# Performance work log

Hardware: AMD Instinct MI355X
Metric: run time of the kernel (lower is better)

## Reference

```python
import jax, jax.numpy as jnp
import numpy as np
from jax import lax

STRIDE = 4

def grid_sample_nearest(feat, grid):
    # feat: (B, C, H, W); grid: (B, Ho, Wo, 2) normalized to [-1, 1], align_corners=True,
    # mode='nearest', padding_mode='zeros' (matches torch.nn.functional.grid_sample).
    B, C, H, W = feat.shape
    gx = (grid[..., 0] + 1.0) * 0.5 * (W - 1)
    gy = (grid[..., 1] + 1.0) * 0.5 * (H - 1)
    ix = jnp.round(gx).astype(jnp.int32)  # round-half-to-even == std::nearbyint
    iy = jnp.round(gy).astype(jnp.int32)
    valid = (ix >= 0) & (ix < W) & (iy >= 0) & (iy < H)
    ixc = jnp.clip(ix, 0, W - 1)
    iyc = jnp.clip(iy, 0, H - 1)
    out = jax.vmap(lambda f, y, x: f[:, y, x])(feat, iyc, ixc)  # (B, C, Ho, Wo)
    return out * valid[:, None, :, :].astype(feat.dtype)

def unfold_s(x, s):
    # F.unfold(x, kernel=(s,s), stride=s): (n,c,h,w) -> (n, c*s*s, h//s * w//s)
    n, c, h, w = x.shape
    h4, w4 = h // s, w // s
    x = x.reshape(n, c, h4, s, w4, s).transpose(0, 1, 3, 5, 2, 4)  # (n,c,kh,kw,h4,w4)
    return x.reshape(n, c * s * s, h4 * w4)

def fold_s(x, s, c, h, w):
    # F.fold, kernel=(s,s), stride=s (non-overlapping): (n, c*s*s, h4*w4) -> (n,c,h,w)
    n = x.shape[0]
    h4, w4 = h // s, w // s
    x = x.reshape(n, c, s, s, h4, w4).transpose(0, 1, 4, 2, 5, 3)  # (n,c,h4,kh,w4,kw)
    return x.reshape(n, c, h, w)

def _normalize(x, axis):
    return x / jnp.maximum(jnp.linalg.norm(x, axis=axis, keepdims=True), 1e-12)

def ltam_forward(curr_feat, index_feat_set_s1, anchor_feat, sparse_feat_set_s1,
                 sparse_feat_set_s2, sparse_feat_set_s3, location_feat,
                 fusion_w, fusion_b):
    s = STRIDE
    n, c, h, w = anchor_feat.shape
    t = sparse_feat_set_s1.shape[1]
    h4, w4 = h // s, w // s
    feat_len = c * s * s
    feat_num = h4 * w4

    # build normalized nearest-sampling grid from location map
    gf = location_feat.reshape(n, t, 2, h4, w4).transpose(0, 1, 3, 4, 2)  # (n,t,h4,w4,2)
    gx = 2.0 * gf[..., 0] / max(w4 - 1, 1) - 1.0
    gy = 2.0 * gf[..., 1] / max(h4 - 1, 1) - 1.0
    grid = jnp.stack([gx, gy], axis=-1).reshape(n * t, h4, w4, 2)

    def warp(fs):
        return grid_sample_nearest(fs.reshape(n * t, feat_len, h4, w4), grid)

    out_s1 = warp(sparse_feat_set_s1)   # (n*t, feat_len, h4, w4)
    out_s2 = warp(sparse_feat_set_s2)
    out_s3 = warp(sparse_feat_set_s3)
    idx_s1 = warp(index_feat_set_s1)

    # current-frame patch tokens, L2-normalized
    cf = unfold_s(curr_feat, s).transpose(0, 2, 1)          # (n, feat_num, feat_len)
    cf = _normalize(cf, axis=2)

    # index tokens per frame, L2-normalized, correlate with current tokens
    idx_tok = idx_s1.reshape(n, t, feat_len, feat_num).transpose(0, 3, 1, 2)  # (n,feat_num,t,feat_len)
    idx_tok = _normalize(idx_tok, axis=3)
    matrix_index = jnp.einsum('nptf,npf->npt', idx_tok, cf)  # (n, feat_num, t)

    corr_soft = jnp.max(matrix_index, axis=2)                # (n, feat_num)
    corr_index = jnp.argmax(matrix_index, axis=2)            # (n, feat_num)

    corr_soft_map = fold_s(jnp.broadcast_to(corr_soft[:, None, :], (n, feat_len, feat_num)),
                           s, c, h, w)                       # (n, c, h, w)

    def gather_fold(o):
        o = o.reshape(n, t, feat_len, feat_num)
        idx = jnp.broadcast_to(corr_index[:, None, None, :], (n, 1, feat_len, feat_num))
        g = jnp.take_along_axis(o, idx, axis=1)[:, 0]        # (n, feat_len, feat_num)
        return fold_s(g, s, c, h, w)

    f1 = gather_fold(out_s1)
    f2 = gather_fold(out_s2)
    f3 = gather_fold(out_s3)

    out = jnp.concatenate([f1, f2, f3], axis=1)              # (n, 3c, h, w)
    out = lax.conv_general_dilated(out, fusion_w, (1, 1), ((1, 1), (1, 1)),
                                   dimension_numbers=('NCHW', 'OIHW', 'NCHW'))
    out = out + fusion_b[None, :, None, None]
    out = out * corr_soft_map + anchor_feat
    return out

def setup_inputs() -> dict:
    key = jax.random.key(0)
    ks = jax.random.split(key, 10)
    n, t, c, h, w, s = 1, 4, 128, 192, 192, STRIDE
    h4, w4 = h // s, w // s
    feat_len = c * s * s
    inp = {
        'curr_feat': jax.random.normal(ks[0], (n, c, h, w), jnp.float32),
        'index_feat_set_s1': jax.random.normal(ks[1], (n, t, feat_len, h4, w4), jnp.float32),
        'anchor_feat': jax.random.normal(ks[2], (n, c, h, w), jnp.float32),
        'sparse_feat_set_s1': jax.random.normal(ks[3], (n, t, feat_len, h4, w4), jnp.float32),
        'sparse_feat_set_s2': jax.random.normal(ks[4], (n, t, feat_len, h4, w4), jnp.float32),
        'sparse_feat_set_s3': jax.random.normal(ks[5], (n, t, feat_len, h4, w4), jnp.float32),
        # unnormalized pixel coordinates in [0, dim-1] (h4 == w4 here)
        'location_feat': jax.random.uniform(ks[6], (n, 2 * t, h4, w4), jnp.float32) * (w4 - 1),
        'fusion_w': jax.random.normal(ks[7], (c, 3 * c, 3, 3), jnp.float32) * 0.02,
        'fusion_b': jax.random.normal(ks[8], (c,), jnp.float32) * 0.02,
    }
    return inp

def reference(curr_feat, index_feat_set_s1, anchor_feat, sparse_feat_set_s1,
              sparse_feat_set_s2, sparse_feat_set_s3, location_feat,
              fusion_w, fusion_b):
    return ltam_forward(curr_feat, index_feat_set_s1, anchor_feat, sparse_feat_set_s1,
                        sparse_feat_set_s2, sparse_feat_set_s3, location_feat,
                        fusion_w, fusion_b)
```

## Files before the change

kernel.cpp:

```cpp
#include <hip/hip_runtime.h>
#include <hip/hip_bf16.h>
#include <math.h>

#define T_FRAMES 4
#define C 128
#define H 192
#define W 192
#define H4 48
#define W4 48
#define FEAT_LEN 2048
#define FEAT_NUM 2304
#define HW (H*W)
#define NCH 384
#define KTOT 3456
#define NSTEP 54
#define PPX 194

typedef __bf16 bf16x8 __attribute__((ext_vector_type(8)));
typedef float f32x4 __attribute__((ext_vector_type(4)));

__device__ __forceinline__ void gl16(const void* gp, void* ldsbase) {
    __builtin_amdgcn_global_load_lds(
        (const __attribute__((address_space(1))) void*)gp,
        (__attribute__((address_space(3))) void*)ldsbase, 16, 0, 0);
}

__device__ __forceinline__ void sample_loc(const float* __restrict__ loc, int k, int p,
                                           int& iy, int& ix, int& valid) {
    float gfx = loc[(2*k+0)*FEAT_NUM + p];
    float gfy = loc[(2*k+1)*FEAT_NUM + p];
    float gx = 2.0f*gfx/47.0f - 1.0f;
    float gy = 2.0f*gfy/47.0f - 1.0f;
    float fx = (gx + 1.0f)*0.5f*47.0f;
    float fy = (gy + 1.0f)*0.5f*47.0f;
    int jx = (int)rintf(fx);
    int jy = (int)rintf(fy);
    valid = (jx >= 0 && jx < W4 && jy >= 0 && jy < H4) ? 1 : 0;
    ix = min(max(jx, 0), W4-1);
    iy = min(max(jy, 0), H4-1);
}

__global__ __launch_bounds__(256) void k_tr(const float* __restrict__ src,
                                            float* __restrict__ dst) {
    __shared__ float lds[64*65];
    int p0 = blockIdx.x*64, f0 = blockIdx.y*64, k = blockIdx.z;
    const float* s = src + (size_t)k*FEAT_LEN*FEAT_NUM;
    float* d = dst + (size_t)k*FEAT_NUM*FEAT_LEN;
    int tid = threadIdx.x;
    int pq = (tid & 15)*4, fr = tid >> 4;
#pragma unroll
    for (int i = 0; i < 4; ++i) {
        int fl = fr + i*16;
        float4 v = *(const float4*)&s[(size_t)(f0+fl)*FEAT_NUM + p0 + pq];
        lds[fl*65 + pq + 0] = v.x;
        lds[fl*65 + pq + 1] = v.y;
        lds[fl*65 + pq + 2] = v.z;
        lds[fl*65 + pq + 3] = v.w;
    }
    __syncthreads();
    int f4 = (tid & 15)*4, pb = tid >> 4;
#pragma unroll
    for (int i = 0; i < 4; ++i) {
        int pl2 = pb + i*16;
        float4 v = { lds[(f4+0)*65 + pl2], lds[(f4+1)*65 + pl2],
                     lds[(f4+2)*65 + pl2], lds[(f4+3)*65 + pl2] };
        *(float4*)&d[(size_t)(p0+pl2)*FEAT_LEN + f0 + f4] = v;
    }
}

__global__ __launch_bounds__(256) void k_trs(const float* __restrict__ s1,
                                             const float* __restrict__ s2,
                                             const float* __restrict__ s3,
                                             ushort* __restrict__ spT) {
    __shared__ float lds[64*65];
    int p0 = blockIdx.x*64, f0 = blockIdx.y*64;
    int z = blockIdx.z;
    int set = z >> 2, k = z & 3;
    const float* src = (set == 0) ? s1 : ((set == 1) ? s2 : s3);
    const float* s = src + (size_t)k*FEAT_LEN*FEAT_NUM;
    int tid = threadIdx.x;
    int pq = (tid & 15)*4, fr = tid >> 4;
#pragma unroll
    for (int i = 0; i < 4; ++i) {
        int fl = fr + i*16;
        float4 v = *(const float4*)&s[(size_t)(f0+fl)*FEAT_NUM + p0 + pq];
        lds[fl*65 + pq + 0] = v.x;
        lds[fl*65 + pq + 1] = v.y;
        lds[fl*65 + pq + 2] = v.z;
        lds[fl*65 + pq + 3] = v.w;
    }
    __syncthreads();
    int fo = (tid & 7)*8, pr = tid >> 3;
#pragma unroll
    for (int i = 0; i < 2; ++i) {
        int row = pr + i*32;
        ushort vv[8];
#pragma unroll
        for (int j = 0; j < 8; ++j) {
            __hip_bfloat16 b = __float2bfloat16(lds[(fo+j)*65 + row]);
            vv[j] = *(ushort*)&b;
        }
        uint4 pk;
        pk.x = (uint)vv[0] | ((uint)vv[1] << 16);
        pk.y = (uint)vv[2] | ((uint)vv[3] << 16);
        pk.z = (uint)vv[4] | ((uint)vv[5] << 16);
        pk.w = (uint)vv[6] | ((uint)vv[7] << 16);
        *(uint4*)(spT + ((size_t)z*FEAT_NUM + p0 + row)*FEAT_LEN + f0 + fo) = pk;
    }
}

__global__ __launch_bounds__(256) void k_gather2(const ushort* __restrict__ spT,
                                                 const float* __restrict__ loc,
                                                 const int* __restrict__ corr_index,
                                                 ushort* __restrict__ cat) {
    __shared__ ushort tok[3*FEAT_LEN];
    int p = blockIdx.x;
    int y4 = p / W4, x4 = p - y4*W4;
    int tid = threadIdx.x;
    int k = corr_index[p];
    int iy, ix, valid;
    sample_loc(loc, k, p, iy, ix, valid);
    int sp = iy*W4 + ix;

#pragma unroll
    for (int j = 0; j < 3; ++j) {
        int idx = j*256 + tid;
        int set = idx >> 8, off = (idx & 255)*8;
        uint4 v = {0u,0u,0u,0u};
        if (valid)
            v = *(const uint4*)(spT + ((size_t)(set*4 + k)*FEAT_NUM + sp)*FEAT_LEN + off);
        *(uint4*)(tok + set*FEAT_LEN + off) = v;
    }
    __syncthreads();

#pragma unroll
    for (int j = 0; j < 3; ++j) {
        int idx = j*256 + tid;
        int px16 = idx / 48, oct = idx - px16*48;
        int ky = px16 >> 2, kx = px16 & 3;
        int y = y4*4 + ky, x = x4*4 + kx;
        int set = oct >> 4, c0 = (oct & 15)*8;
        int sub = (ky << 2) + kx;
        ushort vv[8];
#pragma unroll
        for (int e = 0; e < 8; ++e) vv[e] = tok[set*FEAT_LEN + ((c0 + e) << 4) + sub];
        uint4 pk;
        pk.x = (uint)vv[0] | ((uint)vv[1] << 16);
        pk.y = (uint)vv[2] | ((uint)vv[3] << 16);
        pk.z = (uint)vv[4] | ((uint)vv[5] << 16);
        pk.w = (uint)vv[6] | ((uint)vv[7] << 16);
        *(uint4*)(cat + ((size_t)(y+1)*PPX + (x+1))*NCH + set*128 + c0) = pk;
    }
}

__global__ __launch_bounds__(256) void k_corr2(const float* __restrict__ curr,
                                               const float* __restrict__ idxT,
                                               const float* __restrict__ loc,
                                               int* __restrict__ corr_index,
                                               float* __restrict__ corr_soft) {
    int p = blockIdx.x;
    int y4 = p / W4, x4 = p - y4*W4;
    int tid = threadIdx.x;

    int iy[T_FRAMES], ix[T_FRAMES], valid[T_FRAMES];
    const float* tok[T_FRAMES];
#pragma unroll
    for (int k = 0; k < T_FRAMES; ++k) {
        sample_loc(loc, k, p, iy[k], ix[k], valid[k]);
        tok[k] = idxT + ((size_t)k*FEAT_NUM + iy[k]*W4 + ix[k])*FEAT_LEN;
    }

    float ss_cf = 0.f;
    float dotk[T_FRAMES] = {0.f,0.f,0.f,0.f};
    float ssk[T_FRAMES]  = {0.f,0.f,0.f,0.f};
    int ybase = y4*4, xbase = x4*4;

#pragma unroll
    for (int it = 0; it < 2; ++it) {
        int f4 = (tid + it*256)*4;
        int cc = f4 >> 4, kh = (f4 >> 2) & 3;
        float4 cf = *(const float4*)&curr[cc*HW + (ybase+kh)*W + xbase];
        ss_cf += cf.x*cf.x + cf.y*cf.y + cf.z*cf.z + cf.w*cf.w;
#pragma unroll
        for (int k = 0; k < T_FRAMES; ++k) {
            if (valid[k]) {
                float4 v = *(const float4*)&tok[k][f4];
                dotk[k] += cf.x*v.x + cf.y*v.y + cf.z*v.z + cf.w*v.w;
                ssk[k]  += v.x*v.x + v.y*v.y + v.z*v.z + v.w*v.w;
            }
        }
    }

    float vals[9] = {ss_cf, dotk[0],dotk[1],dotk[2],dotk[3], ssk[0],ssk[1],ssk[2],ssk[3]};
#pragma unroll
    for (int j = 0; j < 9; ++j) {
        float v = vals[j];
#pragma unroll
        for (int off = 32; off > 0; off >>= 1) v += __shfl_xor(v, off, 64);
        vals[j] = v;
    }
    __shared__ float red[4][9];
    int wave = tid >> 6, lane = tid & 63;
    if (lane == 0) {
#pragma unroll
        for (int j = 0; j < 9; ++j) red[wave][j] = vals[j];
    }
    __syncthreads();
    if (tid == 0) {
        float tot[9];
#pragma unroll
        for (int j = 0; j < 9; ++j) tot[j] = red[0][j]+red[1][j]+red[2][j]+red[3][j];
        float ncf = fmaxf(sqrtf(tot[0]), 1e-12f);
        float best = -1e30f; int bestk = 0;
#pragma unroll
        for (int k = 0; k < T_FRAMES; ++k) {
            float nk = fmaxf(sqrtf(tot[5+k]), 1e-12f);
            float m = tot[1+k] / (nk * ncf);
            if (m > best) { best = m; bestk = k; }
        }
        corr_index[p] = bestk;
        corr_soft[p]  = best;
    }
}

__global__ __launch_bounds__(256) void k_corr(const float* __restrict__ curr,
                                              const float* __restrict__ idxf,
                                              const float* __restrict__ loc,
                                              int* __restrict__ corr_index,
                                              float* __restrict__ corr_soft) {
    int p = blockIdx.x;
    int y4 = p / W4, x4 = p - y4*W4;
    int tid = threadIdx.x;

    int iy[T_FRAMES], ix[T_FRAMES], valid[T_FRAMES];
#pragma unroll
    for (int k = 0; k < T_FRAMES; ++k) sample_loc(loc, k, p, iy[k], ix[k], valid[k]);

    float ss_cf = 0.f;
    float dotk[T_FRAMES] = {0.f,0.f,0.f,0.f};
    float ssk[T_FRAMES]  = {0.f,0.f,0.f,0.f};

    int ybase = y4*4, xbase = x4*4;
    for (int f = tid; f < FEAT_LEN; f += 256) {
        int cc = f >> 4;
        int kh = (f >> 2) & 3;
        int kw = f & 3;
        float cf = curr[cc*HW + (ybase+kh)*W + (xbase+kw)];
        ss_cf += cf*cf;
#pragma unroll
        for (int k = 0; k < T_FRAMES; ++k) {
            float v = 0.f;
            if (valid[k]) v = idxf[(k*FEAT_LEN + f)*FEAT_NUM + iy[k]*W4 + ix[k]];
            dotk[k] += cf*v;
            ssk[k]  += v*v;
        }
    }

    float vals[9] = {ss_cf, dotk[0],dotk[1],dotk[2],dotk[3], ssk[0],ssk[1],ssk[2],ssk[3]};
#pragma unroll
    for (int j = 0; j < 9; ++j) {
        float v = vals[j];
#pragma unroll
        for (int off = 32; off > 0; off >>= 1) v += __shfl_xor(v, off, 64);
        vals[j] = v;
    }
    __shared__ float red[4][9];
    int wave = tid >> 6, lane = tid & 63;
    if (lane == 0) {
#pragma unroll
        for (int j = 0; j < 9; ++j) red[wave][j] = vals[j];
    }
    __syncthreads();
    if (tid == 0) {
        float tot[9];
#pragma unroll
        for (int j = 0; j < 9; ++j) tot[j] = red[0][j]+red[1][j]+red[2][j]+red[3][j];
        float ncf = fmaxf(sqrtf(tot[0]), 1e-12f);
        float best = -1e30f; int bestk = 0;
#pragma unroll
        for (int k = 0; k < T_FRAMES; ++k) {
            float nk = fmaxf(sqrtf(tot[5+k]), 1e-12f);
            float m = tot[1+k] / (nk * ncf);
            if (m > best) { best = m; bestk = k; }
        }
        corr_index[p] = bestk;
        corr_soft[p]  = best;
    }
}

__global__ __launch_bounds__(256) void k_wconv(const float* __restrict__ w,
                                               ushort* __restrict__ wt2) {
    int gid = blockIdx.x*256 + threadIdx.x;
    if (gid >= 128*KTOT) return;
    int e  = gid & 7;
    int l  = (gid >> 3) & 63;
    int g  = (gid >> 9) & 7;
    int kkstep = gid >> 12;
    int kk = kkstep & 1, step = kkstep >> 1;
    int lx = l & 15, lg = l >> 4;
    int col = g*16 + lx;
    int chunk = step / 9, tap = step - chunk*9;
    int ci = chunk*64 + kk*32 + lg*8 + e;
    __hip_bfloat16 b = __float2bfloat16(w[(col*NCH + ci)*9 + tap]);
    wt2[gid] = *(ushort*)&b;
}

__global__ __launch_bounds__(256) void k_border(ushort* __restrict__ cat) {
    int gid = blockIdx.x*256 + threadIdx.x;
    if (gid >= 772*48) return;
    int oct = gid % 48, bp = gid / 48;
    int ypad, xpad;
    if (bp < 194)      { ypad = 0;        xpad = bp; }
    else if (bp < 388) { ypad = 193;      xpad = bp - 194; }
    else if (bp < 580) { ypad = bp - 387; xpad = 0; }
    else               { ypad = bp - 579; xpad = 193; }
    uint4 z = {0u,0u,0u,0u};
    *(uint4*)(cat + (ypad*PPX + xpad)*NCH + oct*8) = z;
}

__global__ __launch_bounds__(256) void k_gather(const float* __restrict__ s1,
                                                const float* __restrict__ s2,
                                                const float* __restrict__ s3,
                                                const float* __restrict__ loc,
                                                const int* __restrict__ corr_index,
                                                ushort* __restrict__ cat) {
    int gid = blockIdx.x*256 + threadIdx.x;
    if (gid >= HW*48) return;
    int oct = gid % 48, px = gid / 48;
    int x = px % W, y = px / W;
    int p = (y >> 2)*W4 + (x >> 2);
    int k = corr_index[p];
    int iy, ix, valid;
    sample_loc(loc, k, p, iy, ix, valid);
    int set = oct >> 4;
    int c0  = (oct & 15) * 8;
    int sub = ((y & 3) << 2) + (x & 3);
    ushort v[8];
#pragma unroll
    for (int e = 0; e < 8; ++e) v[e] = 0;
    if (valid) {
        const float* src = (set == 0) ? s1 : ((set == 1) ? s2 : s3);
        const float* sp = src + (size_t)k*FEAT_LEN*FEAT_NUM + iy*W4 + ix;
#pragma unroll
        for (int e = 0; e < 8; ++e) {
            int f = ((c0 + e) << 4) + sub;
            __hip_bfloat16 b = __float2bfloat16(sp[(size_t)f*FEAT_NUM]);
            v[e] = *(ushort*)&b;
        }
    }
    uint4 pk;
    pk.x = (uint)v[0] | ((uint)v[1] << 16);
    pk.y = (uint)v[2] | ((uint)v[3] << 16);
    pk.z = (uint)v[4] | ((uint)v[5] << 16);
    pk.w = (uint)v[6] | ((uint)v[7] << 16);
    *(uint4*)(cat + ((y+1)*PPX + (x+1))*NCH + oct*8) = pk;
}

__global__ __launch_bounds__(256, 2) void k_conv2(const ushort* __restrict__ cat,
                                                  const ushort* __restrict__ wt2,
                                                  const float* __restrict__ bias,
                                                  const float* __restrict__ corr_soft,
                                                  const float* __restrict__ anchor,
                                                  float* __restrict__ out) {
    __shared__ char smX[2][136*128];

    int tx = blockIdx.x, ty = blockIdx.y;
    int tid = threadIdx.x;
    int wave = tid >> 6, l = tid & 63;
    int lx = l & 15, lg = l >> 4;
    int co0w = wave * 32;
    int wbofs = (wave*64)*16;

    auto stageX = [&](int chunk, int b) {
        char* xb = (char*)smX[b];
#pragma unroll
        for (int q = 0; q < 4; ++q) {
            int idx = tid + q*256;
            int rc = idx >> 3, oct = idx & 7;
            int r = rc / 34, xp = rc - r*34;
            int octp = oct ^ (xp & 7);
            const ushort* gp = cat + ((size_t)(ty*2 + r)*PPX + (tx*32 + xp))*NCH
                               + chunk*64 + octp*8;
            gl16(gp, xb + q*256*16 + wbofs);
        }
        if (wave == 0) {
            int idx = 1024 + l;
            int rc = idx >> 3, oct = idx & 7;
            int xp = rc - 102;
            int octp = oct ^ (xp & 7);
            const ushort* gp = cat + ((size_t)(ty*2 + 3)*PPX + (tx*32 + xp))*NCH
                               + chunk*64 + octp*8;
            gl16(gp, xb + 1024*16);
        }
    };

    f32x4 acc[2][4];
#pragma unroll
    for (int mf = 0; mf < 2; ++mf)
#pragma unroll
        for (int nf = 0; nf < 4; ++nf) acc[mf][nf] = (f32x4){0.f,0.f,0.f,0.f};

    int pyv[4], pxxv[4];
#pragma unroll
    for (int nf = 0; nf < 4; ++nf) { int pxl = nf*16 + lx; pyv[nf] = pxl >> 5; pxxv[nf] = pxl & 31; }
    const ushort* wfb[2];
#pragma unroll
    for (int mf = 0; mf < 2; ++mf)
        wfb[mf] = wt2 + ((wave*2 + mf)*64 + l)*8;

    stageX(0, 0);
    __syncthreads();

    for (int chunk = 0; chunk < 6; ++chunk) {
        if (chunk < 5) stageX(chunk+1, (chunk+1) & 1);
        const char* Xb = smX[chunk & 1];
#pragma unroll
        for (int tap = 0; tap < 9; ++tap) {
            const int step = chunk*9 + tap;
            const int dy = tap/3 - 1, dx = tap%3 - 1;
            bf16x8 wf[2][2];
#pragma unroll
            for (int mf = 0; mf < 2; ++mf)
#pragma unroll
                for (int kk = 0; kk < 2; ++kk)
                    wf[mf][kk] = *(const bf16x8*)(wfb[mf] + (size_t)(step*2 + kk)*4096);
            int xrc[4], xsw[4];
#pragma unroll
            for (int nf = 0; nf < 4; ++nf) {
                int xp2 = pxxv[nf] + dx + 1;
                xrc[nf] = (pyv[nf] + dy + 1)*34 + xp2;
                xsw[nf] = (xp2 & 7) << 4;
            }
#pragma unroll
            for (int kk = 0; kk < 2; ++kk) {
                int kb = kk*64 + lg*16;
                bf16x8 xf[4];
#pragma unroll
                for (int nf = 0; nf < 4; ++nf)
                    xf[nf] = *(const bf16x8*)(Xb + xrc[nf]*128 + (kb ^ xsw[nf]));
#pragma unroll
                for (int mf = 0; mf < 2; ++mf)
#pragma unroll
                    for (int nf = 0; nf < 4; ++nf)
                        acc[mf][nf] = __builtin_amdgcn_mfma_f32_16x16x32_bf16(
                            wf[mf][kk], xf[nf], acc[mf][nf], 0, 0, 0);
            }
        }
        __syncthreads();
    }

    float cs[4]; int pixo[4];
#pragma unroll
    for (int nf = 0; nf < 4; ++nf) {
        int y = ty*2 + pyv[nf];
        int x = tx*32 + pxxv[nf];
        cs[nf] = corr_soft[(ty >> 1)*W4 + (x >> 2)];
        pixo[nf] = y*W + x;
    }
#pragma unroll
    for (int mf = 0; mf < 2; ++mf) {
#pragma unroll
        for (int j = 0; j < 4; ++j) {
            int co = co0w + mf*16 + lg*4 + j;
            float b = bias[co];
#pragma unroll
            for (int nf = 0; nf < 4; ++nf) {
                int o = co*HW + pixo[nf];
                out[o] = (acc[mf][nf][j] + b)*cs[nf] + anchor[o];
            }
        }
    }
}

extern "C" void kernel_launch(void* const* d_in, const int* in_sizes, int n_in,
                              void* d_out, int out_size, void* d_ws, size_t ws_size,
                              hipStream_t stream) {
    const float* curr   = (const float*)d_in[0];
    const float* idxf   = (const float*)d_in[1];
    const float* anchor = (const float*)d_in[2];
    const float* s1     = (const float*)d_in[3];
    const float* s2     = (const float*)d_in[4];
    const float* s3     = (const float*)d_in[5];
    const float* loc    = (const float*)d_in[6];
    const float* wgt    = (const float*)d_in[7];
    const float* bias   = (const float*)d_in[8];
    float* out = (float*)d_out;

    char* ws = (char*)d_ws;
    int*    corr_index = (int*)ws;
    float*  corr_soft  = (float*)(ws + 16384);
    ushort* wt2        = (ushort*)(ws + 32768);
    ushort* cat        = (ushort*)(ws + 917504);
    char*   big        = ws + 917504 + 28912128;
    float*  idxT       = (float*)big;
    ushort* spT        = (ushort*)big;
    const size_t SPT_BYTES  = (size_t)3*T_FRAMES*FEAT_NUM*FEAT_LEN*2;
    const size_t IDXT_BYTES = (size_t)T_FRAMES*FEAT_NUM*FEAT_LEN*4;
    const size_t NEED_A = 29829632 + (SPT_BYTES > IDXT_BYTES ? SPT_BYTES : IDXT_BYTES);
    const size_t NEED_B = 917504 + IDXT_BYTES;

    if (ws_size >= NEED_A) {
        hipLaunchKernelGGL(k_tr, dim3(36, 32, 4), dim3(256), 0, stream, idxf, idxT);
        hipLaunchKernelGGL(k_corr2, dim3(FEAT_NUM), dim3(256), 0, stream,
                           curr, idxT, loc, corr_index, corr_soft);
        hipLaunchKernelGGL(k_wconv, dim3((128*KTOT + 255)/256), dim3(256), 0, stream, wgt, wt2);
        hipLaunchKernelGGL(k_border, dim3((772*48 + 255)/256), dim3(256), 0, stream, cat);
        hipLaunchKernelGGL(k_trs, dim3(36, 32, 12), dim3(256), 0, stream, s1, s2, s3, spT);
        hipLaunchKernelGGL(k_gather2, dim3(FEAT_NUM), dim3(256), 0, stream,
                           spT, loc, corr_index, cat);
    } else {
        float*  idxT_b = (float*)(ws + 917504);
        ushort* cat_b  = (ushort*)(ws + 917504);
        if (ws_size >= NEED_B) {
            hipLaunchKernelGGL(k_tr, dim3(36, 32, 4), dim3(256), 0, stream, idxf, idxT_b);
            hipLaunchKernelGGL(k_corr2, dim3(FEAT_NUM), dim3(256), 0, stream,
                               curr, idxT_b, loc, corr_index, corr_soft);
        } else {
            hipLaunchKernelGGL(k_corr, dim3(FEAT_NUM), dim3(256), 0, stream,
                               curr, idxf, loc, corr_index, corr_soft);
        }
        hipLaunchKernelGGL(k_wconv, dim3((128*KTOT + 255)/256), dim3(256), 0, stream, wgt, wt2);
        hipLaunchKernelGGL(k_border, dim3((772*48 + 255)/256), dim3(256), 0, stream, cat_b);
        hipLaunchKernelGGL(k_gather, dim3((HW*48 + 255)/256), dim3(256), 0, stream,
                           s1, s2, s3, loc, corr_index, cat_b);
        hipLaunchKernelGGL(k_conv2, dim3(6, 96), dim3(256), 0, stream,
                           cat_b, wt2, bias, corr_soft, anchor, out);
        return;
    }
    hipLaunchKernelGGL(k_conv2, dim3(6, 96), dim3(256), 0, stream,
                       cat, wt2, bias, corr_soft, anchor, out);
}
```

Before: 202.6 us.

## Skip transposing feature rows that no sampling location references

A small kernel builds a per-frame bitmask of which source positions the nearest-sample grid actually hits. The correlation kernel records a second bitmask for the winning frame's positions. Both transpose kernels then skip writing rows whose position is not marked, which cuts global write traffic for the transposed index and sparse-feature buffers. This costs a memset, an extra tiny launch and atomics, and source reads still happen in full.

```diff
diff --git a/kernel.cpp b/kernel.cpp
--- a/kernel.cpp
+++ b/kernel.cpp
@@ -15,6 +15,7 @@
 #define KTOT 3456
 #define NSTEP 54
 #define PPX 194
+#define NBW 72
 
 typedef __bf16 bf16x8 __attribute__((ext_vector_type(8)));
 typedef float f32x4 __attribute__((ext_vector_type(4)));
@@ -40,8 +41,22 @@
     iy = min(max(jy, 0), H4-1);
 }
 
+__global__ __launch_bounds__(256) void k_needA(const float* __restrict__ loc,
+                                               uint* __restrict__ needA) {
+    int p = blockIdx.x*256 + threadIdx.x;
+    if (p >= FEAT_NUM) return;
+#pragma unroll
+    for (int k = 0; k < T_FRAMES; ++k) {
+        int iy, ix, valid;
+        sample_loc(loc, k, p, iy, ix, valid);
+        int sp = iy*W4 + ix;
+        atomicOr(&needA[k*NBW + (sp >> 5)], 1u << (sp & 31));
+    }
+}
+
 __global__ __launch_bounds__(256) void k_tr(const float* __restrict__ src,
-                                            float* __restrict__ dst) {
+                                            float* __restrict__ dst,
+                                            const uint* __restrict__ needA) {
     __shared__ float lds[64*65];
     int p0 = blockIdx.x*64, f0 = blockIdx.y*64, k = blockIdx.z;
     const float* s = src + (size_t)k*FEAT_LEN*FEAT_NUM;
@@ -62,16 +77,19 @@
 #pragma unroll
     for (int i = 0; i < 4; ++i) {
         int pl2 = pb + i*16;
+        int sp = p0 + pl2;
+        if (!(needA[k*NBW + (sp >> 5)] & (1u << (sp & 31)))) continue;
         float4 v = { lds[(f4+0)*65 + pl2], lds[(f4+1)*65 + pl2],
                      lds[(f4+2)*65 + pl2], lds[(f4+3)*65 + pl2] };
-        *(float4*)&d[(size_t)(p0+pl2)*FEAT_LEN + f0 + f4] = v;
+        *(float4*)&d[(size_t)sp*FEAT_LEN + f0 + f4] = v;
     }
 }
 
 __global__ __launch_bounds__(256) void k_trs(const float* __restrict__ s1,
                                              const float* __restrict__ s2,
                                              const float* __restrict__ s3,
-                                             ushort* __restrict__ spT) {
+                                             ushort* __restrict__ spT,
+                                             const uint* __restrict__ needB) {
     __shared__ float lds[64*65];
     int p0 = blockIdx.x*64, f0 = blockIdx.y*64;
     int z = blockIdx.z;
@@ -94,6 +112,8 @@
 #pragma unroll
     for (int i = 0; i < 2; ++i) {
         int row = pr + i*32;
+        int sp = p0 + row;
+        if (!(needB[k*NBW + (sp >> 5)] & (1u << (sp & 31)))) continue;
         ushort vv[8];
 #pragma unroll
         for (int j = 0; j < 8; ++j) {
@@ -105,7 +125,7 @@
         pk.y = (uint)vv[2] | ((uint)vv[3] << 16);
         pk.z = (uint)vv[4] | ((uint)vv[5] << 16);
         pk.w = (uint)vv[6] | ((uint)vv[7] << 16);
-        *(uint4*)(spT + ((size_t)z*FEAT_NUM + p0 + row)*FEAT_LEN + f0 + fo) = pk;
+        *(uint4*)(spT + ((size_t)z*FEAT_NUM + sp)*FEAT_LEN + f0 + fo) = pk;
     }
 }
 
@@ -157,7 +177,8 @@
                                                const float* __restrict__ idxT,
                                                const float* __restrict__ loc,
                                                int* __restrict__ corr_index,
-                                               float* __restrict__ corr_soft) {
+                                               float* __restrict__ corr_soft,
+                                               uint* __restrict__ needB) {
     int p = blockIdx.x;
     int y4 = p / W4, x4 = p - y4*W4;
     int tid = threadIdx.x;
@@ -220,6 +241,8 @@
         }
         corr_index[p] = bestk;
         corr_soft[p]  = best;
+        int spb = iy[bestk]*W4 + ix[bestk];
+        atomicOr(&needB[bestk*NBW + (spb >> 5)], 1u << (spb & 31));
     }
 }
 
@@ -488,6 +511,8 @@
 
     char* ws = (char*)d_ws;
     int*    corr_index = (int*)ws;
+    uint*   needA      = (uint*)(ws + 12288);
+    uint*   needB      = (uint*)(ws + 13696);
     float*  corr_soft  = (float*)(ws + 16384);
     ushort* wt2        = (ushort*)(ws + 32768);
     ushort* cat        = (ushort*)(ws + 917504);
@@ -500,21 +525,26 @@
     const size_t NEED_B = 917504 + IDXT_BYTES;
 
     if (ws_size >= NEED_A) {
-        hipLaunchKernelGGL(k_tr, dim3(36, 32, 4), dim3(256), 0, stream, idxf, idxT);
+        hipMemsetAsync(ws + 12288, 0, 2560, stream);
+        hipLaunchKernelGGL(k_needA, dim3(9), dim3(256), 0, stream, loc, needA);
+        hipLaunchKernelGGL(k_tr, dim3(36, 32, 4), dim3(256), 0, stream, idxf, idxT, needA);
         hipLaunchKernelGGL(k_corr2, dim3(FEAT_NUM), dim3(256), 0, stream,
-                           curr, idxT, loc, corr_index, corr_soft);
+                           curr, idxT, loc, corr_index, corr_soft, needB);
         hipLaunchKernelGGL(k_wconv, dim3((128*KTOT + 255)/256), dim3(256), 0, stream, wgt, wt2);
         hipLaunchKernelGGL(k_border, dim3((772*48 + 255)/256), dim3(256), 0, stream, cat);
-        hipLaunchKernelGGL(k_trs, dim3(36, 32, 12), dim3(256), 0, stream, s1, s2, s3, spT);
+        hipLaunchKernelGGL(k_trs, dim3(36, 32, 12), dim3(256), 0, stream,
+                           s1, s2, s3, spT, needB);
         hipLaunchKernelGGL(k_gather2, dim3(FEAT_NUM), dim3(256), 0, stream,
                            spT, loc, corr_index, cat);
     } else {
         float*  idxT_b = (float*)(ws + 917504);
         ushort* cat_b  = (ushort*)(ws + 917504);
         if (ws_size >= NEED_B) {
-            hipLaunchKernelGGL(k_tr, dim3(36, 32, 4), dim3(256), 0, stream, idxf, idxT_b);
+            hipMemsetAsync(ws + 12288, 0, 2560, stream);
+            hipLaunchKernelGGL(k_needA, dim3(9), dim3(256), 0, stream, loc, needA);
+            hipLaunchKernelGGL(k_tr, dim3(36, 32, 4), dim3(256), 0, stream, idxf, idxT_b, needA);
             hipLaunchKernelGGL(k_corr2, dim3(FEAT_NUM), dim3(256), 0, stream,
-                               curr, idxT_b, loc, corr_index, corr_soft);
+                               curr, idxT_b, loc, corr_index, corr_soft, needB);
         } else {
             hipLaunchKernelGGL(k_corr, dim3(FEAT_NUM), dim3(256), 0, stream,
                                curr, idxf, loc, corr_index, corr_soft);
```

New measurement: 203.2 us. About the same (+0.3%).
